# Kernel tuning notes

Hardware: AMD Instinct MI355X
Metric: run time of the kernel (lower is better)

Reference implementation:

```python
import jax, jax.numpy as jnp
import numpy as np

N_VERTICES = 24  # hardcoded via torch.eye(24) in the original
K = 3


def normalized_adj(adj):
    # scipy version: L = (A @ D^-1/2).T @ D^-1/2 = D^-1/2 @ A^T @ D^-1/2
    d = adj.sum(axis=1)
    d_inv_sqrt = jnp.where(d > 0, 1.0 / jnp.sqrt(d), 0.0)
    return (adj * d_inv_sqrt[None, :]).T * d_inv_sqrt[None, :]


def cheb_polynomials(L, k_order):
    Ts = [jnp.eye(N_VERTICES, dtype=L.dtype), L]
    for _ in range(2, k_order):
        Ts.append(2.0 * L @ Ts[-1] - Ts[-2])
    return jnp.stack(Ts[:k_order])  # (K, N, N)


def setup_inputs() -> dict:
    key = jax.random.key(0)
    k1, k2, k3 = jax.random.split(key, 3)
    x = jax.random.normal(k1, (64, 32, N_VERTICES, 512), dtype=jnp.float32)
    adj = jax.random.uniform(k2, (N_VERTICES, N_VERTICES), dtype=jnp.float32)
    Theta = jax.random.normal(k3, (K, 32, 32), dtype=jnp.float32)
    return {"x": x, "adj": adj, "Theta": Theta}


def reference(x, adj, Theta):
    # x: (b, c, n, t); adj: (n, n); Theta: (K, c, o)
    L = normalized_adj(adj)
    T = cheb_polynomials(L, K)  # (K, n, m)
    # original per-timestep, per-k: rhs[b,m,c] = sum_n x[b,n,c] T_k[n,m];
    # out[b,m,o] += rhs @ Theta_k. Fused over t and k, final permute -> (b,o,m,t).
    out = jnp.einsum('knm,bcnt,kco->bomt', T, x, Theta)
    return out
```

## Files before the change

kernel.cpp:

```cpp
#include <hip/hip_runtime.h>
#include <hip/hip_bf16.h>
#include <stdint.h>


#define NV 24
#define CIN 32
#define COUT 32
#define TDIM 512
#define BATCH 64
#define MDIM 768
#define KD 768
#define BM 128
#define BN 128
#define BK 32
#define NKT (KD / BK)
#define NTT (TDIM / BN)
#define NMT (MDIM / BM)
#define BLOB (BM * BK)
#define BSTRIDE 40

typedef __attribute__((ext_vector_type(8))) short short8v;
typedef __attribute__((ext_vector_type(4))) float float4v;

__device__ inline unsigned short f2bf(float f) {
    unsigned int u = __float_as_uint(f);
    unsigned int r = (u + 0x7fffu + ((u >> 16) & 1u)) >> 16;
    return (unsigned short)r;
}

__global__ __launch_bounds__(256) void prep_w(const float* __restrict__ adj,
                                              const float* __restrict__ Theta,
                                              unsigned short* __restrict__ Wp) {
    __shared__ float adjS[NV * NV];
    __shared__ float disS[NV];
    __shared__ float LS[NV * NV];
    __shared__ float T2S[NV * NV];
    int tid = threadIdx.x;
    for (int e = tid; e < NV * NV; e += 256) adjS[e] = adj[e];
    __syncthreads();
    if (tid < NV) {
        float d = 0.f;
        for (int j = 0; j < NV; ++j) d += adjS[tid * NV + j];
        disS[tid] = (d > 0.f) ? rsqrtf(d) : 0.f;
    }
    __syncthreads();
    for (int e = tid; e < NV * NV; e += 256) {
        int i = e / NV, j = e % NV;
        LS[e] = disS[i] * adjS[j * NV + i] * disS[j];
    }
    __syncthreads();
    for (int e = tid; e < NV * NV; e += 256) {
        int i = e / NV, j = e % NV;
        float s = 0.f;
        for (int p = 0; p < NV; ++p) s += LS[i * NV + p] * LS[p * NV + j];
        T2S[e] = 2.f * s - (i == j ? 1.f : 0.f);
    }
    __syncthreads();
    int r0 = blockIdx.x * (MDIM / 64);
    for (int e = tid; e < (MDIM / 64) * KD; e += 256) {
        int lr = e / KD, col = e % KD;
        int row = r0 + lr;
        int o = row / NV, m = row % NV;
        int c = col / NV, n = col % NV;
        float th0 = Theta[0 * CIN * COUT + c * COUT + o];
        float th1 = Theta[1 * CIN * COUT + c * COUT + o];
        float th2 = Theta[2 * CIN * COUT + c * COUT + o];
        float v = (n == m ? th0 : 0.f) + LS[n * NV + m] * th1 + T2S[n * NV + m] * th2;
        size_t idx = (((size_t)(row >> 7) * NKT + (col >> 5)) * BM + (row & 127)) * BK + (col & 31);
        Wp[idx] = f2bf(v);
    }
}

__global__ __launch_bounds__(256, 4) void gemm_fused(const unsigned short* __restrict__ Wp,
                                                     const float* __restrict__ x,
                                                     float* __restrict__ out) {
    __shared__ __attribute__((aligned(16))) unsigned short As[BM * BK];
    __shared__ __attribute__((aligned(16))) unsigned short Bs[BN * BSTRIDE];

    int id = blockIdx.x;
    int hi = id / 48;
    int rem = id - hi * 48;
    int mt = rem >> 3;
    int g = hi * 8 + (rem & 7);
    int b = g >> 2;
    int tt = g & 3;

    int tid = threadIdx.x;
    int wave = tid >> 6;
    int lane = tid & 63;
    int quad = lane >> 4;
    int l16 = lane & 15;
    int wm = wave >> 1, wn = wave & 1;
    int kq = wave;
    int tp = lane;

    const unsigned short* Ab = Wp + (size_t)mt * NKT * BLOB;
    const float* xb = x + (size_t)b * KD * TDIM + tt * BN;

    const float4v zero4 = {0.f, 0.f, 0.f, 0.f};
    float4v acc[4][4];
#pragma unroll
    for (int i = 0; i < 4; ++i)
#pragma unroll
        for (int j = 0; j < 4; ++j) acc[i][j] = zero4;

    uint4 Ar0, Ar1;
    float Xr[16];

    {
        const uint4* ap = (const uint4*)Ab;
        Ar0 = ap[tid];
        Ar1 = ap[tid + 256];
        const float* xr = xb + (size_t)(kq * 8) * TDIM;
#pragma unroll
        for (int kk = 0; kk < 8; ++kk) {
            Xr[kk] = xr[(size_t)kk * TDIM + tp];
            Xr[8 + kk] = xr[(size_t)kk * TDIM + tp + 64];
        }
    }

    for (int kt = 0; kt < NKT; ++kt) {
        union { short8v s; __hip_bfloat162 h[4]; } u0, u1;
#pragma unroll
        for (int i = 0; i < 4; ++i) {
            u0.h[i] = __float22bfloat162_rn({Xr[2 * i], Xr[2 * i + 1]});
            u1.h[i] = __float22bfloat162_rn({Xr[8 + 2 * i], Xr[8 + 2 * i + 1]});
        }
        uint4 a0 = Ar0, a1 = Ar1;

        __syncthreads();
        *(uint4*)(As + tid * 8) = a0;
        *(uint4*)(As + 2048 + tid * 8) = a1;
        *(short8v*)(Bs + tp * BSTRIDE + kq * 8) = u0.s;
        *(short8v*)(Bs + (tp + 64) * BSTRIDE + kq * 8) = u1.s;
        __syncthreads();

        if (kt + 1 < NKT) {
            const uint4* ap = (const uint4*)(Ab + (size_t)(kt + 1) * BLOB);
            Ar0 = ap[tid];
            Ar1 = ap[tid + 256];
            const float* xr = xb + (size_t)((kt + 1) * BK + kq * 8) * TDIM;
#pragma unroll
            for (int kk = 0; kk < 8; ++kk) {
                Xr[kk] = xr[(size_t)kk * TDIM + tp];
                Xr[8 + kk] = xr[(size_t)kk * TDIM + tp + 64];
            }
        }

        short8v a[4], bb[4];
#pragma unroll
        for (int i = 0; i < 4; ++i)
            a[i] = *(const short8v*)(As + (wm * 64 + i * 16 + l16) * BK + quad * 8);
#pragma unroll
        for (int j = 0; j < 4; ++j)
            bb[j] = *(const short8v*)(Bs + (wn * 64 + j * 16 + l16) * BSTRIDE + quad * 8);
#pragma unroll
        for (int i = 0; i < 4; ++i)
#pragma unroll
            for (int j = 0; j < 4; ++j)
                acc[i][j] = __builtin_amdgcn_mfma_f32_16x16x32_bf16(a[i], bb[j], acc[i][j], 0, 0, 0);
    }

    float* outB = out + (size_t)b * MDIM * TDIM;
    int rbase = mt * BM + wm * 64;
    int cbase = tt * BN + wn * 64;
#pragma unroll
    for (int i = 0; i < 4; ++i) {
#pragma unroll
        for (int j = 0; j < 4; ++j) {
            int row0 = rbase + i * 16 + quad * 4;
            int col = cbase + j * 16 + l16;
#pragma unroll
            for (int r = 0; r < 4; ++r)
                outB[(size_t)(row0 + r) * TDIM + col] = acc[i][j][r];
        }
    }
}

extern "C" void kernel_launch(void* const* d_in, const int* in_sizes, int n_in,
                              void* d_out, int out_size, void* d_ws, size_t ws_size,
                              hipStream_t stream) {
    const float* x = (const float*)d_in[0];
    const float* adj = (const float*)d_in[1];
    const float* Theta = (const float*)d_in[2];
    float* out = (float*)d_out;

    unsigned short* Wp = (unsigned short*)d_ws;

    prep_w<<<64, 256, 0, stream>>>(adj, Theta, Wp);
    gemm_fused<<<NMT * NTT * BATCH, 256, 0, stream>>>(Wp, x, out);
}
```

Measured before the change: 221.0 us.

## Double-buffer B tile, load A fragments directly to registers, swizzle LDS

The A (weight) operand no longer goes through shared memory: each wave loads its MFMA fragments straight from the pre-packed global layout into registers, double-buffered even/odd. The B tile from x is double-buffered in LDS with an XOR swizzle instead of padding, and x is prefetched two k-steps ahead. This leaves one barrier per k-step instead of two. Output stores become nontemporal, and the occupancy hint drops from 4 to 3 blocks per SM to make room for the extra registers.

```diff
diff --git a/kernel.cpp b/kernel.cpp
--- a/kernel.cpp
+++ b/kernel.cpp
@@ -17,10 +17,12 @@
 #define NTT (TDIM / BN)
 #define NMT (MDIM / BM)
 #define BLOB (BM * BK)
-#define BSTRIDE 40
+#define BSH (BN * BK)
 
 typedef __attribute__((ext_vector_type(8))) short short8v;
 typedef __attribute__((ext_vector_type(4))) float float4v;
+
+union PackU { short8v s; __hip_bfloat162 h[4]; };
 
 __device__ inline unsigned short f2bf(float f) {
     unsigned int u = __float_as_uint(f);
@@ -71,11 +73,46 @@
     }
 }
 
-__global__ __launch_bounds__(256, 4) void gemm_fused(const unsigned short* __restrict__ Wp,
+#define STEP(KT, BUF, XC, AC, AN)                                              \
+    do {                                                                       \
+        PackU u0, u1;                                                          \
+        _Pragma("unroll")                                                      \
+        for (int i = 0; i < 4; ++i) {                                          \
+            u0.h[i] = __float22bfloat162_rn({XC[2 * i], XC[2 * i + 1]});       \
+            u1.h[i] = __float22bfloat162_rn({XC[8 + 2 * i], XC[8 + 2 * i + 1]}); \
+        }                                                                      \
+        *(short8v*)(Bs + (BUF) * BSH + wr0) = u0.s;                            \
+        *(short8v*)(Bs + (BUF) * BSH + wr0 + 64 * BK) = u1.s;                  \
+        if ((KT) + 1 < NKT) {          \
+            const short8v* Ap_ = (const short8v*)(Ab + (size_t)((KT) + 1) * BLOB); \
+            _Pragma("unroll")                                                  \
+            for (int i = 0; i < 4; ++i) AN[i] = Ap_[afr + i * 64];             \
+        }                                                                      \
+        if ((KT) + 2 < NKT) {  \
+            const float* xr_ = xb + (size_t)(((KT) + 2) * BK + kq * 8) * TDIM; \
+            _Pragma("unroll")                                                  \
+            for (int kk = 0; kk < 8; ++kk) {                                   \
+                XC[kk] = xr_[(size_t)kk * TDIM + tp];                          \
+                XC[8 + kk] = xr_[(size_t)kk * TDIM + tp + 64];                 \
+            }                                                                  \
+        }                                                                      \
+        __syncthreads();  \
+        short8v bb[4];                                                         \
+        _Pragma("unroll")                                                      \
+        for (int j = 0; j < 4; ++j)                                            \
+            bb[j] = *(const short8v*)(Bs + (BUF) * BSH + rb + j * (16 * BK));  \
+        _Pragma("unroll")                                                      \
+        for (int i = 0; i < 4; ++i)                                            \
+            _Pragma("unroll")                                                  \
+            for (int j = 0; j < 4; ++j)                                        \
+                acc[i][j] = __builtin_amdgcn_mfma_f32_16x16x32_bf16(           \
+                    AC[i], bb[j], acc[i][j], 0, 0, 0);                         \
+    } while (0)
+
+__global__ __launch_bounds__(256, 3) void gemm_fused(const unsigned short* __restrict__ Wp,
                                                      const float* __restrict__ x,
                                                      float* __restrict__ out) {
-    __shared__ __attribute__((aligned(16))) unsigned short As[BM * BK];
-    __shared__ __attribute__((aligned(16))) unsigned short Bs[BN * BSTRIDE];
+    __shared__ __attribute__((aligned(16))) unsigned short Bs[2 * BSH];
 
     int id = blockIdx.x;
     int hi = id / 48;
@@ -97,6 +134,10 @@
     const unsigned short* Ab = Wp + (size_t)mt * NKT * BLOB;
     const float* xb = x + (size_t)b * KD * TDIM + tt * BN;
 
+    int wr0 = (tp * BK + kq * 8) ^ ((tp & 7) * 8);
+    int rb = ((wn * 64 + l16) * BK + quad * 8) ^ ((l16 & 7) * 8);
+    int afr = (wm * 64 + l16) * 4 + quad;
+
     const float4v zero4 = {0.f, 0.f, 0.f, 0.f};
     float4v acc[4][4];
 #pragma unroll
@@ -104,61 +145,30 @@
 #pragma unroll
         for (int j = 0; j < 4; ++j) acc[i][j] = zero4;
 
-    uint4 Ar0, Ar1;
-    float Xr[16];
+    float XrA[16], XrB[16];
+    short8v Aev[4], Aod[4];
 
     {
-        const uint4* ap = (const uint4*)Ab;
-        Ar0 = ap[tid];
-        Ar1 = ap[tid + 256];
         const float* xr = xb + (size_t)(kq * 8) * TDIM;
 #pragma unroll
         for (int kk = 0; kk < 8; ++kk) {
-            Xr[kk] = xr[(size_t)kk * TDIM + tp];
-            Xr[8 + kk] = xr[(size_t)kk * TDIM + tp + 64];
+            XrA[kk] = xr[(size_t)kk * TDIM + tp];
+            XrA[8 + kk] = xr[(size_t)kk * TDIM + tp + 64];
         }
-    }
-
-    for (int kt = 0; kt < NKT; ++kt) {
-        union { short8v s; __hip_bfloat162 h[4]; } u0, u1;
-#pragma unroll
-        for (int i = 0; i < 4; ++i) {
-            u0.h[i] = __float22bfloat162_rn({Xr[2 * i], Xr[2 * i + 1]});
-            u1.h[i] = __float22bfloat162_rn({Xr[8 + 2 * i], Xr[8 + 2 * i + 1]});
+        const short8v* Ap = (const short8v*)Ab;
+#pragma unroll
+        for (int i = 0; i < 4; ++i) Aev[i] = Ap[afr + i * 64];
+        const float* xr1 = xb + (size_t)(BK + kq * 8) * TDIM;
+#pragma unroll
+        for (int kk = 0; kk < 8; ++kk) {
+            XrB[kk] = xr1[(size_t)kk * TDIM + tp];
+            XrB[8 + kk] = xr1[(size_t)kk * TDIM + tp + 64];
         }
-        uint4 a0 = Ar0, a1 = Ar1;
-
-        __syncthreads();
-        *(uint4*)(As + tid * 8) = a0;
-        *(uint4*)(As + 2048 + tid * 8) = a1;
-        *(short8v*)(Bs + tp * BSTRIDE + kq * 8) = u0.s;
-        *(short8v*)(Bs + (tp + 64) * BSTRIDE + kq * 8) = u1.s;
-        __syncthreads();
-
-        if (kt + 1 < NKT) {
-            const uint4* ap = (const uint4*)(Ab + (size_t)(kt + 1) * BLOB);
-            Ar0 = ap[tid];
-            Ar1 = ap[tid + 256];
-            const float* xr = xb + (size_t)((kt + 1) * BK + kq * 8) * TDIM;
-#pragma unroll
-            for (int kk = 0; kk < 8; ++kk) {
-                Xr[kk] = xr[(size_t)kk * TDIM + tp];
-                Xr[8 + kk] = xr[(size_t)kk * TDIM + tp + 64];
-            }
-        }
-
-        short8v a[4], bb[4];
-#pragma unroll
-        for (int i = 0; i < 4; ++i)
-            a[i] = *(const short8v*)(As + (wm * 64 + i * 16 + l16) * BK + quad * 8);
-#pragma unroll
-        for (int j = 0; j < 4; ++j)
-            bb[j] = *(const short8v*)(Bs + (wn * 64 + j * 16 + l16) * BSTRIDE + quad * 8);
-#pragma unroll
-        for (int i = 0; i < 4; ++i)
-#pragma unroll
-            for (int j = 0; j < 4; ++j)
-                acc[i][j] = __builtin_amdgcn_mfma_f32_16x16x32_bf16(a[i], bb[j], acc[i][j], 0, 0, 0);
+    }
+
+    for (int kt = 0; kt < NKT; kt += 2) {
+        STEP(kt, 0, XrA, Aev, Aod);
+        STEP(kt + 1, 1, XrB, Aod, Aev);
     }
 
     float* outB = out + (size_t)b * MDIM * TDIM;
@@ -172,7 +182,8 @@
             int col = cbase + j * 16 + l16;
 #pragma unroll
             for (int r = 0; r < 4; ++r)
-                outB[(size_t)(row0 + r) * TDIM + col] = acc[i][j][r];
+                __builtin_nontemporal_store(acc[i][j][r],
+                                            &outB[(size_t)(row0 + r) * TDIM + col]);
         }
     }
 }
```

After: 233.7 us. 1.06x slower.

## Pre-pack x to bf16 fragment layout and load MFMA operands directly

Applied to the files above, without the earlier changes.

Adds an xprep kernel that converts x to bf16 and transposes it into a K-tiled layout that matches the MFMA fragments. A new GEMM kernel then reads A and B fragments straight from global memory, with no LDS staging and no __syncthreads. This removes the in-loop fp32-to-bf16 conversion, the shared-memory round trip and the barriers. In exchange it adds a separate pass over x that writes a bf16 copy, and the GEMM loop loses explicit prefetching. The old path remains as a fallback when the workspace is too small.

```diff
diff --git a/kernel.cpp b/kernel.cpp
--- a/kernel.cpp
+++ b/kernel.cpp
@@ -17,7 +17,10 @@
 #define NTT (TDIM / BN)
 #define NMT (MDIM / BM)
 #define BLOB (BM * BK)
-#define BSTRIDE 40
+
+#define WP_SHORTS ((size_t)NMT * NKT * BLOB)
+#define XP_SHORTS ((size_t)BATCH * NKT * TDIM * BK)
+#define WS_NEED ((WP_SHORTS + XP_SHORTS) * 2)
 
 typedef __attribute__((ext_vector_type(8))) short short8v;
 typedef __attribute__((ext_vector_type(4))) float float4v;
@@ -71,9 +74,111 @@
     }
 }
 
-__global__ __launch_bounds__(256, 4) void gemm_fused(const unsigned short* __restrict__ Wp,
-                                                     const float* __restrict__ x,
-                                                     float* __restrict__ out) {
+#define TSTR 132
+__global__ __launch_bounds__(256) void xprep(const float* __restrict__ x,
+                                             unsigned short* __restrict__ xp) {
+    __shared__ float LS[BK * TSTR];
+    int bid = blockIdx.x;
+    int tc = bid & 3;
+    int kt = (bid >> 2) % NKT;
+    int b = bid / (NKT * 4);
+    int tid = threadIdx.x;
+    int w = tid >> 6;
+    int lane = tid & 63;
+    int hi2 = lane >> 5;
+    int tl = lane & 31;
+
+    const float* xs = x + ((size_t)b * KD + kt * BK) * TDIM + tc * 128;
+    float4 v[4];
+#pragma unroll
+    for (int c = 0; c < 4; ++c) {
+        int k = w * 8 + c * 2 + hi2;
+        v[c] = *(const float4*)(xs + (size_t)k * TDIM + tl * 4);
+    }
+#pragma unroll
+    for (int c = 0; c < 4; ++c) {
+        int k = w * 8 + c * 2 + hi2;
+        *(float4*)(&LS[k * TSTR + tl * 4]) = v[c];
+    }
+    __syncthreads();
+    int t = tid >> 1, kh = tid & 1;
+    union { short8v s[2]; __hip_bfloat162 h[8]; } u;
+#pragma unroll
+    for (int p = 0; p < 8; ++p) {
+        float f0 = LS[(kh * 16 + 2 * p) * TSTR + t];
+        float f1 = LS[(kh * 16 + 2 * p + 1) * TSTR + t];
+        u.h[p] = __float22bfloat162_rn({f0, f1});
+    }
+    unsigned short* xd = xp + (((size_t)b * NKT + kt) * TDIM + tc * 128 + t) * BK + kh * 16;
+    *(short8v*)(xd) = u.s[0];
+    *(short8v*)(xd + 8) = u.s[1];
+}
+
+__global__ __launch_bounds__(256, 4) void gemm_direct(const unsigned short* __restrict__ Wp,
+                                                      const unsigned short* __restrict__ xp,
+                                                      float* __restrict__ out) {
+    int id = blockIdx.x;
+    int hi = id / 48;
+    int rem = id - hi * 48;
+    int mt = rem >> 3;
+    int g = hi * 8 + (rem & 7);
+    int b = g >> 2;
+    int tt = g & 3;
+
+    int tid = threadIdx.x;
+    int wave = tid >> 6;
+    int lane = tid & 63;
+    int quad = lane >> 4;
+    int l16 = lane & 15;
+    int wm = wave >> 1, wn = wave & 1;
+
+    const short8v* Ap = (const short8v*)(Wp) + (size_t)mt * NKT * (BLOB / 8);
+    const short8v* Bp = (const short8v*)(xp) + ((size_t)b * NKT * TDIM + (size_t)tt * BN) * (BK / 8);
+    int afr = (wm * 64 + l16) * 4 + quad;
+    int bfr = (wn * 64 + l16) * 4 + quad;
+
+    const float4v zero4 = {0.f, 0.f, 0.f, 0.f};
+    float4v acc[4][4];
+#pragma unroll
+    for (int i = 0; i < 4; ++i)
+#pragma unroll
+        for (int j = 0; j < 4; ++j) acc[i][j] = zero4;
+
+    for (int kt = 0; kt < NKT; ++kt) {
+        short8v a[4], bb[4];
+#pragma unroll
+        for (int i = 0; i < 4; ++i) a[i] = Ap[afr + i * 64];
+#pragma unroll
+        for (int j = 0; j < 4; ++j) bb[j] = Bp[bfr + j * 64];
+#pragma unroll
+        for (int i = 0; i < 4; ++i)
+#pragma unroll
+            for (int j = 0; j < 4; ++j)
+                acc[i][j] = __builtin_amdgcn_mfma_f32_16x16x32_bf16(a[i], bb[j], acc[i][j], 0, 0, 0);
+        Ap += BLOB / 8;
+        Bp += TDIM * BK / 8;
+    }
+
+    float* outB = out + (size_t)b * MDIM * TDIM;
+    int rbase = mt * BM + wm * 64;
+    int cbase = tt * BN + wn * 64;
+#pragma unroll
+    for (int i = 0; i < 4; ++i) {
+#pragma unroll
+        for (int j = 0; j < 4; ++j) {
+            int row0 = rbase + i * 16 + quad * 4;
+            int col = cbase + j * 16 + l16;
+#pragma unroll
+            for (int r = 0; r < 4; ++r)
+                outB[(size_t)(row0 + r) * TDIM + col] = acc[i][j][r];
+        }
+    }
+}
+
+#define BSTRIDE 40
+__global__ __launch_bounds__(256, 4) void gemm_fallback(const unsigned short* __restrict__ Wp,
+                                                        const float* __restrict__ x,
+                                                        float* __restrict__ out) {
     __shared__ __attribute__((aligned(16))) unsigned short As[BM * BK];
     __shared__ __attribute__((aligned(16))) unsigned short Bs[BN * BSTRIDE];
 
@@ -106,7 +211,6 @@
 
     uint4 Ar0, Ar1;
     float Xr[16];
-
     {
         const uint4* ap = (const uint4*)Ab;
         Ar0 = ap[tid];
@@ -188,5 +292,11 @@
     unsigned short* Wp = (unsigned short*)d_ws;
 
     prep_w<<<64, 256, 0, stream>>>(adj, Theta, Wp);
-    gemm_fused<<<NMT * NTT * BATCH, 256, 0, stream>>>(Wp, x, out);
-}
+    if (ws_size >= WS_NEED) {
+        unsigned short* xp = Wp + WP_SHORTS;
+        xprep<<<BATCH * NKT * 4, 256, 0, stream>>>(x, xp);
+        gemm_direct<<<NMT * NTT * BATCH, 256, 0, stream>>>(Wp, xp, out);
+    } else {
+        gemm_fallback<<<NMT * NTT * BATCH, 256, 0, stream>>>(Wp, x, out);
+    }
+}
```

Measured after the change: 251.2 us. +13.7%, slower.
